# Optimization experiments

Measured on AMD Instinct MI355X. Metric: run time of the kernel, lower is better.

Reference implementation:

```python
import jax, jax.numpy as jnp
import numpy as np

NUM_HEADS = 8

def setup_inputs() -> dict:
    key = jax.random.key(0)
    ks = jax.random.split(key, 16)
    B, N, M, C = 4, 2048, 2048, 256
    Hd = 4 * C  # mlp hidden = dim * mlp_ratio
    std = 0.02
    x = jax.random.normal(ks[0], (B, N, C), dtype=jnp.float32)
    y = jax.random.normal(ks[1], (B, M, C), dtype=jnp.float32)
    token_types = jax.random.randint(ks[2], (B, N), 0, 2).astype(jnp.int64)
    token_types = token_types.at[0, 0].set(0)  # take the fresh-kv branch
    inp = {
        'x': x, 'y': y, 'token_types': token_types,
        'Wq': jax.random.normal(ks[3], (C, C)) * std,
        'Wkv': jax.random.normal(ks[4], (C, 2 * C)) * std,
        'Ws1': jax.random.normal(ks[5], (C, Hd)) * std,
        'bs1': jnp.zeros((Hd,)),
        'Ws2': jax.random.normal(ks[6], (Hd, C)) * std,
        'bs2': jnp.zeros((C,)),
        'Wl1': jax.random.normal(ks[7], (C, Hd)) * std,
        'bl1': jnp.zeros((Hd,)),
        'Wl2': jax.random.normal(ks[8], (Hd, C)) * std,
        'bl2': jnp.zeros((C,)),
    }
    return inp


def reference(x, y, token_types, Wq, Wkv, Ws1, bs1, Ws2, bs2, Wl1, bl1, Wl2, bl2):
    B, N, C = x.shape
    H = NUM_HEADS
    d = C // H
    scale = d ** -0.5
    # q: [B,H,N,d]
    q = (x @ Wq).reshape(B, N, H, d).transpose(0, 2, 1, 3)
    # kv: [B,M,2,H,d] -> k,v: [B,H,M,d]
    M = y.shape[1]
    kv = (y @ Wkv).reshape(B, M, 2, H, d)
    k = kv[:, :, 0].transpose(0, 2, 1, 3)
    v = kv[:, :, 1].transpose(0, 2, 1, 3)
    attn = jax.nn.softmax(jnp.einsum('bhnd,bhmd->bhnm', q, k) * scale, axis=-1)
    ctx = jnp.einsum('bhnm,bhmd->bhnd', attn, v)  # [B,H,N,d]
    ctx = ctx.transpose(0, 2, 1, 3).reshape(B, N, C)
    # MoE MLP: expert_s for token_type==0, expert_l for token_type==1
    out_s = jax.nn.gelu(ctx @ Ws1 + bs1, approximate=False) @ Ws2 + bs2
    out_l = jax.nn.gelu(ctx @ Wl1 + bl1, approximate=False) @ Wl2 + bl2
    is_l = (token_types == 1)[..., None]
    out = jnp.where(is_l, out_l, out_s)
    return out
```

## Files before the change

### kernel.cpp

```cpp
#include <hip/hip_runtime.h>

typedef unsigned short ushort_t;
typedef __attribute__((ext_vector_type(8))) short bf16x8;
typedef __attribute__((ext_vector_type(4))) short bf16x4;
typedef __attribute__((ext_vector_type(4))) float f32x4;

#define MFMA16(a, b, c) __builtin_amdgcn_mfma_f32_16x16x32_bf16(a, b, c, 0, 0, 0)

typedef const __attribute__((address_space(1))) void gvoid_t;
typedef __attribute__((address_space(3))) void lvoid_t;

__device__ __forceinline__ void glds16(const ushort_t* g, ushort_t* l) {
    __builtin_amdgcn_global_load_lds((gvoid_t*)(const void*)g, (lvoid_t*)(void*)l, 16, 0, 0);
}

__device__ inline ushort_t f2bf(float f) {
    union { float f; unsigned int i; } v;
    v.f = f;
    unsigned int r = v.i + 0x7FFFu + ((v.i >> 16) & 1u);
    return (ushort_t)(r >> 16);
}

__device__ __forceinline__ unsigned int cvtpk_bf16(float lo, float hi) {
    unsigned int r;
    asm("v_cvt_pk_bf16_f32 %0, %1, %2" : "=v"(r) : "v"(lo), "v"(hi));
    return r;
}

__device__ __forceinline__ float fexp2(float x) {
    float r;
    asm("v_exp_f32 %0, %1" : "=v"(r) : "v"(x));
    return r;
}

__device__ __forceinline__ float gelu_fast(float x) {
    float z = x * 0.70710678118654752f;
    float a = fabsf(z);
    float den = 1.0f + 0.3275911f * a;
    float tr;
    asm("v_rcp_f32 %0, %1" : "=v"(tr) : "v"(den));
    float poly = ((((1.061405429f * tr - 1.453152027f) * tr + 1.421413741f) * tr
                   - 0.284496736f) * tr + 0.254829592f) * tr;
    float e = fexp2(-z * z * 1.4426950408889634f);
    float erfa = 1.0f - poly * e;
    float erfv = copysignf(erfa, z);
    return 0.5f * x * (1.0f + erfv);
}

__global__ __launch_bounds__(256) void prep_k(
    const float* Wq, const float* Wkv, const float* Ws1,
    const float* Ws2, const float* Wl1, const float* Wl2,
    const float* x, const float* y, const int* tt,
    ushort_t* WqT, ushort_t* WkvT, ushort_t* Ws1T,
    ushort_t* Ws2T, ushort_t* Wl1T, ushort_t* Wl2T,
    ushort_t* xb, ushort_t* yb,
    int* perm0, int* perm1, int* cnt)
{
    const int job = blockIdx.y;
    const int t = threadIdx.x;
    if (job < 6) {
        __shared__ ushort_t lds[64][65];
        const float* src; ushort_t* dst; int R, Cc;
        switch (job) {
            case 0:  src = Wq;  dst = WqT;  R = 256;  Cc = 256;  break;
            case 1:  src = Wkv; dst = WkvT; R = 256;  Cc = 512;  break;
            case 2:  src = Ws1; dst = Ws1T; R = 256;  Cc = 1024; break;
            case 3:  src = Ws2; dst = Ws2T; R = 1024; Cc = 256;  break;
            case 4:  src = Wl1; dst = Wl1T; R = 256;  Cc = 1024; break;
            default: src = Wl2; dst = Wl2T; R = 1024; Cc = 256;  break;
        }
        const int ctiles = Cc >> 6;
        const int ntiles = (R >> 6) * ctiles;
        for (int tile = blockIdx.x; tile < ntiles; tile += gridDim.x) {
            const int r0 = (tile / ctiles) << 6, c0 = (tile - (tile / ctiles) * ctiles) << 6;
            #pragma unroll
            for (int it = 0; it < 16; ++it) {
                int idx = it * 256 + t;
                int rr = idx >> 6, cc = idx & 63;
                lds[rr][cc] = f2bf(src[(size_t)(r0 + rr) * Cc + c0 + cc]);
            }
            __syncthreads();
            #pragma unroll
            for (int it = 0; it < 16; ++it) {
                int idx = it * 256 + t;
                int rr = idx >> 6, cc = idx & 63;
                dst[(size_t)(c0 + rr) * R + r0 + cc] = lds[cc][rr];
            }
            __syncthreads();
        }
    } else if (job < 8) {
        const float* src = (job == 6) ? x : y;
        ushort_t* dst = (job == 6) ? xb : yb;
        const int tid = blockIdx.x * 256 + t;
        const int nth = gridDim.x * 256;
        for (int i = tid; i < (1 << 18); i += nth) {
            f32x4 a0 = *(const f32x4*)(src + (size_t)i * 8);
            f32x4 a1 = *(const f32x4*)(src + (size_t)i * 8 + 4);
            union { unsigned int u[4]; bf16x8 v; } o;
            o.u[0] = cvtpk_bf16(a0[0], a0[1]);
            o.u[1] = cvtpk_bf16(a0[2], a0[3]);
            o.u[2] = cvtpk_bf16(a1[0], a1[1]);
            o.u[3] = cvtpk_bf16(a1[2], a1[3]);
            *(bf16x8*)(dst + (size_t)i * 8) = o.v;
        }
    } else {
        if (blockIdx.x != 0) return;
        __shared__ int s0[256], s1[256];
        unsigned int mask = 0;
        #pragma unroll
        for (int j = 0; j < 8; ++j) {
            int4 v = *(const int4*)(tt + t * 32 + j * 4);
            mask |= (unsigned int)(v.x & 1) << (j * 4)
                  | (unsigned int)(v.y & 1) << (j * 4 + 1)
                  | (unsigned int)(v.z & 1) << (j * 4 + 2)
                  | (unsigned int)(v.w & 1) << (j * 4 + 3);
        }
        const int c1 = __popc(mask), c0 = 32 - c1;
        s0[t] = c0; s1[t] = c1;
        __syncthreads();
        for (int d = 1; d < 256; d <<= 1) {
            int a0 = 0, a1 = 0;
            if (t >= d) { a0 = s0[t - d]; a1 = s1[t - d]; }
            __syncthreads();
            s0[t] += a0; s1[t] += a1;
            __syncthreads();
        }
        const int tot0 = s0[255], tot1 = s1[255];
        int off0 = s0[t] - c0, off1 = s1[t] - c1;
        #pragma unroll
        for (int j = 0; j < 32; ++j) {
            int row = t * 32 + j;
            if ((mask >> j) & 1) perm1[off1++] = row;
            else                 perm0[off0++] = row;
        }
        for (int i = tot0 + t; i < 8320; i += 256) perm0[i] = 0;
        for (int i = tot1 + t; i < 8320; i += 256) perm1[i] = 0;
        if (t == 0) { cnt[0] = tot0; cnt[1] = tot1; }
    }
}

template<int ACT, int GATHER, int SCATTER, int OUTF32, int VSCATTER>
__device__ __forceinline__ void gemm_body(
    ushort_t* Als, ushort_t* Bls, int vbid,
    const ushort_t* __restrict__ A, const ushort_t* __restrict__ Bt,
    const float* __restrict__ bias, void* __restrict__ Cv,
    const int* __restrict__ perm, const int* __restrict__ ncnt,
    ushort_t* __restrict__ kpk, ushort_t* __restrict__ vpk,
    float oscale, int M, int N, int K, int aRowOff, int outRowOff)
{
    const int t = threadIdx.x;
    const int lane = t & 63, w = t >> 6;
    const int wr = w >> 1, wc = w & 1;
    const int ntn = N >> 7;
    const int mt = vbid / ntn, nt = vbid - mt * ntn;
    const int mbase = mt << 7, nbase = nt << 7;
    const int n16 = lane & 15, g = lane >> 4;

    int ne = M;
    if (GATHER || SCATTER) {
        ne = *ncnt;
        if (mbase >= ne) return;
    }

    int arow[4], skb[4], brow[4];
    #pragma unroll
    for (int j = 0; j < 4; ++j) {
        int p = j * 256 + t;
        int sr = p >> 3;
        skb[j] = (p & 7) ^ (sr & 7);
        brow[j] = sr;
        arow[j] = GATHER ? perm[mbase + sr] : (mbase + sr + aRowOff);
    }

    f32x4 acc[4][4];
    #pragma unroll
    for (int mi = 0; mi < 4; ++mi)
        #pragma unroll
        for (int ni = 0; ni < 4; ++ni) acc[mi][ni] = (f32x4){0.f, 0.f, 0.f, 0.f};

    for (int k0 = 0; k0 < K; k0 += 64) {
        #pragma unroll
        for (int j = 0; j < 4; ++j) {
            glds16(A + (size_t)arow[j] * K + k0 + skb[j] * 8, &Als[(j * 256 + t) * 8]);
            glds16(Bt + (size_t)(nbase + brow[j]) * K + k0 + skb[j] * 8, &Bls[(j * 256 + t) * 8]);
        }
        __syncthreads();
        #pragma unroll
        for (int ks = 0; ks < 2; ++ks) {
            bf16x8 af[4], bfr[4];
            #pragma unroll
            for (int i = 0; i < 4; ++i) {
                const int ar = wr * 64 + i * 16 + n16;
                af[i]  = *(const bf16x8*)&Als[ar * 64 + (((ks << 2) + g) ^ (ar & 7)) * 8];
                const int br = wc * 64 + i * 16 + n16;
                bfr[i] = *(const bf16x8*)&Bls[br * 64 + (((ks << 2) + g) ^ (br & 7)) * 8];
            }
            #pragma unroll
            for (int mi = 0; mi < 4; ++mi)
                #pragma unroll
                for (int ni = 0; ni < 4; ++ni)
                    acc[mi][ni] = MFMA16(af[mi], bfr[ni], acc[mi][ni]);
        }
        __syncthreads();
    }

    float bv[4];
    #pragma unroll
    for (int ni = 0; ni < 4; ++ni)
        bv[ni] = (bias != nullptr) ? bias[nbase + wc * 64 + ni * 16 + n16] : 0.f;

    #pragma unroll
    for (int mi = 0; mi < 4; ++mi) {
        #pragma unroll
        for (int r = 0; r < 4; ++r) {
            const int pos = mbase + wr * 64 + mi * 16 + (g << 2) + r;
            int orow = pos + outRowOff;
            if (GATHER || SCATTER) {
                if (pos >= ne) continue;
                if (SCATTER) orow = perm[pos];
            }
            #pragma unroll
            for (int ni = 0; ni < 4; ++ni) {
                const int col = nbase + wc * 64 + ni * 16 + n16;
                float v = (acc[mi][ni][r] + bv[ni]) * oscale;
                if (ACT) v = gelu_fast(v);
                if (VSCATTER) {
                    const int bb = pos >> 11, mm = pos & 2047;
                    if (col < 256) {
                        const int hh = col >> 5, dd = col & 31;
                        kpk[(size_t)(bb * 8 + hh) * 65536 + (mm >> 6) * 2048
                            + ((mm >> 4) & 3) * 512
                            + (((dd >> 3) * 16 + (mm & 15)) << 3) + (dd & 7)] = f2bf(v);
                    } else {
                        const int hh = (col - 256) >> 5, dd = (col - 256) & 31;
                        const int m31 = mm & 31;
                        vpk[(size_t)(bb * 8 + hh) * 65536 + (mm >> 6) * 2048
                            + (((mm >> 5) & 1) * 2 + (dd >> 4)) * 512
                            + ((((m31 >> 2) & 3) * 16 + (dd & 15)) << 3)
                            + (((m31 >> 4) & 1) << 2) + (m31 & 3)] = f2bf(v);
                    }
                } else {
                    if (OUTF32) ((float*)Cv)[(size_t)orow * N + col] = v;
                    else ((ushort_t*)Cv)[(size_t)orow * N + col] = f2bf(v);
                }
            }
        }
    }
}

__global__ __launch_bounds__(256, 2) void qkv_k(
    const ushort_t* xb, const ushort_t* yb,
    const ushort_t* WqT, const ushort_t* WkvT,
    ushort_t* qws, ushort_t* kpk, ushort_t* vpk, float qscale)
{
    __shared__ ushort_t Als[128 * 64];
    __shared__ ushort_t Bls[128 * 64];
    if (blockIdx.x < 128) {
        gemm_body<0, 0, 0, 0, 0>(Als, Bls, blockIdx.x, xb, WqT, nullptr, qws,
                                 nullptr, nullptr, nullptr, nullptr,
                                 qscale, 8192, 256, 256, 0, 0);
    } else {
        gemm_body<0, 0, 0, 0, 1>(Als, Bls, blockIdx.x - 128, yb, WkvT, nullptr, nullptr,
                                 nullptr, nullptr, kpk, vpk,
                                 1.f, 8192, 512, 256, 0, 0);
    }
}

__global__ __launch_bounds__(256, 2) void mlp1_k(
    const ushort_t* ctx, const ushort_t* Ws1T, const ushort_t* Wl1T,
    const float* bs1, const float* bl1, ushort_t* hws,
    const int* perm0, const int* perm1, const int* cnt)
{
    __shared__ ushort_t Als[128 * 64];
    __shared__ ushort_t Bls[128 * 64];
    const int half = blockIdx.x >> 9, vbid = blockIdx.x & 511;
    const int outOff = half ? cnt[0] : 0;
    gemm_body<1, 1, 0, 0, 0>(Als, Bls, vbid, ctx, half ? Wl1T : Ws1T,
                             half ? bl1 : bs1, hws,
                             half ? perm1 : perm0, cnt + half, nullptr, nullptr,
                             1.f, 8192, 1024, 256, 0, outOff);
}

__global__ __launch_bounds__(256, 2) void mlp2_k(
    const ushort_t* hws, const ushort_t* Ws2T, const ushort_t* Wl2T,
    const float* bs2, const float* bl2, float* out,
    const int* perm0, const int* perm1, const int* cnt)
{
    __shared__ ushort_t Als[128 * 64];
    __shared__ ushort_t Bls[128 * 64];
    const int half = blockIdx.x >> 7, vbid = blockIdx.x & 127;
    const int aOff = half ? cnt[0] : 0;
    gemm_body<0, 0, 1, 1, 0>(Als, Bls, vbid, hws, half ? Wl2T : Ws2T,
                             half ? bl2 : bs2, out,
                             half ? perm1 : perm0, cnt + half, nullptr, nullptr,
                             1.f, 8192, 256, 1024, aOff, 0);
}

__global__ __launch_bounds__(256, 3) void attn_k(
    const ushort_t* __restrict__ q, const ushort_t* __restrict__ kpack,
    const ushort_t* __restrict__ vpack, ushort_t* __restrict__ ctx)
{
    __shared__ ushort_t KV[2][4096];

    const int t = threadIdx.x, lane = t & 63, w = t >> 6;
    const int bid = (blockIdx.x & 7) * 64 + (blockIdx.x >> 3);
    const int tile = bid & 15, bh = bid >> 4, b = bh >> 3, h = bh & 7;
    const int n16 = lane & 15, g = lane >> 4, lk = g << 3;
    const int row0 = tile * 128 + w * 32;

    const ushort_t* qp = q + ((size_t)(b * 2048 + row0 + n16) * 256 + h * 32 + lk);
    const bf16x8 qf0 = *(const bf16x8*)qp;
    const bf16x8 qf1 = *(const bf16x8*)(qp + 16 * 256);

    const ushort_t* kg = kpack + (size_t)bh * 65536 + t * 8;
    const ushort_t* vg = vpack + (size_t)bh * 65536 + t * 8;

    f32x4 a0d0 = {0.f, 0.f, 0.f, 0.f}, a0d1 = {0.f, 0.f, 0.f, 0.f};
    f32x4 a1d0 = {0.f, 0.f, 0.f, 0.f}, a1d1 = {0.f, 0.f, 0.f, 0.f};
    f32x4 den0 = {0.f, 0.f, 0.f, 0.f}, den1 = {0.f, 0.f, 0.f, 0.f};
    const f32x4 zero = {0.f, 0.f, 0.f, 0.f};
    bf16x8 ones;
    #pragma unroll
    for (int e = 0; e < 8; ++e) ones[e] = (short)0x3F80;

    const int kOff = lane * 8;
    const int vOff = 2048 + lane * 8;

    bf16x8 kreg = *(const bf16x8*)kg;
    bf16x8 vreg = *(const bf16x8*)vg;
    *(bf16x8*)&KV[0][t * 8] = kreg;
    *(bf16x8*)&KV[0][2048 + t * 8] = vreg;

    int cur = 0;
    for (int it = 0; it < 32; ++it) {
        __syncthreads();
        if (it + 1 < 32) {
            kreg = *(const bf16x8*)(kg + (size_t)(it + 1) * 2048);
            vreg = *(const bf16x8*)(vg + (size_t)(it + 1) * 2048);
        }

        bf16x8 kf[4], vf[4];
        #pragma unroll
        for (int i = 0; i < 4; ++i) {
            kf[i] = *(const bf16x8*)&KV[cur][kOff + i * 512];
            vf[i] = *(const bf16x8*)&KV[cur][vOff + i * 512];
        }

        f32x4 st0[4], st1[4];
        __builtin_amdgcn_s_setprio(1);
        #pragma unroll
        for (int mt = 0; mt < 4; ++mt) {
            st0[mt] = MFMA16(kf[mt], qf0, zero);
            st1[mt] = MFMA16(kf[mt], qf1, zero);
        }
        __builtin_amdgcn_s_setprio(0);

        float p0[4][4], p1[4][4];
        #pragma unroll
        for (int mt = 0; mt < 4; ++mt) {
            #pragma unroll
            for (int r = 0; r < 4; ++r) {
                p0[mt][r] = fexp2(st0[mt][r]);
                p1[mt][r] = fexp2(st1[mt][r]);
            }
        }

        __builtin_amdgcn_s_setprio(1);
        #pragma unroll
        for (int kpn = 0; kpn < 2; ++kpn) {
            union { unsigned int u[4]; bf16x8 v; } pb0, pb1;
            pb0.u[0] = cvtpk_bf16(p0[2 * kpn][0], p0[2 * kpn][1]);
            pb0.u[1] = cvtpk_bf16(p0[2 * kpn][2], p0[2 * kpn][3]);
            pb0.u[2] = cvtpk_bf16(p0[2 * kpn + 1][0], p0[2 * kpn + 1][1]);
            pb0.u[3] = cvtpk_bf16(p0[2 * kpn + 1][2], p0[2 * kpn + 1][3]);
            pb1.u[0] = cvtpk_bf16(p1[2 * kpn][0], p1[2 * kpn][1]);
            pb1.u[1] = cvtpk_bf16(p1[2 * kpn][2], p1[2 * kpn][3]);
            pb1.u[2] = cvtpk_bf16(p1[2 * kpn + 1][0], p1[2 * kpn + 1][1]);
            pb1.u[3] = cvtpk_bf16(p1[2 * kpn + 1][2], p1[2 * kpn + 1][3]);
            a0d0 = MFMA16(vf[2 * kpn],     pb0.v, a0d0);
            a0d1 = MFMA16(vf[2 * kpn + 1], pb0.v, a0d1);
            a1d0 = MFMA16(vf[2 * kpn],     pb1.v, a1d0);
            a1d1 = MFMA16(vf[2 * kpn + 1], pb1.v, a1d1);
            den0 = MFMA16(ones, pb0.v, den0);
            den1 = MFMA16(ones, pb1.v, den1);
        }
        __builtin_amdgcn_s_setprio(0);

        if (it + 1 < 32) {
            *(bf16x8*)&KV[cur ^ 1][t * 8] = kreg;
            *(bf16x8*)&KV[cur ^ 1][2048 + t * 8] = vreg;
        }
        cur ^= 1;
    }

    const float i0 = 1.f / den0[0], i1 = 1.f / den1[0];
    bf16x4 s00, s01, s10, s11;
    #pragma unroll
    for (int r = 0; r < 4; ++r) {
        s00[r] = (short)f2bf(a0d0[r] * i0);
        s01[r] = (short)f2bf(a0d1[r] * i0);
        s10[r] = (short)f2bf(a1d0[r] * i1);
        s11[r] = (short)f2bf(a1d1[r] * i1);
    }
    ushort_t* op0 = ctx + (size_t)(b * 2048 + row0 + n16) * 256 + h * 32;
    ushort_t* op1 = op0 + 16 * 256;
    *(bf16x4*)(op0 + 4 * g)      = s00;
    *(bf16x4*)(op0 + 16 + 4 * g) = s01;
    *(bf16x4*)(op1 + 4 * g)      = s10;
    *(bf16x4*)(op1 + 16 + 4 * g) = s11;
}

extern "C" void kernel_launch(void* const* d_in, const int* in_sizes, int n_in,
                              void* d_out, int out_size, void* d_ws, size_t ws_size,
                              hipStream_t stream)
{
    const float* x   = (const float*)d_in[0];
    const float* y   = (const float*)d_in[1];
    const int*   tt  = (const int*)d_in[2];
    const float* Wq  = (const float*)d_in[3];
    const float* Wkv = (const float*)d_in[4];
    const float* Ws1 = (const float*)d_in[5];
    const float* bs1 = (const float*)d_in[6];
    const float* Ws2 = (const float*)d_in[7];
    const float* bs2 = (const float*)d_in[8];
    const float* Wl1 = (const float*)d_in[9];
    const float* bl1 = (const float*)d_in[10];
    const float* Wl2 = (const float*)d_in[11];
    const float* bl2 = (const float*)d_in[12];
    float* out = (float*)d_out;
    ushort_t* ws = (ushort_t*)d_ws;

    ushort_t* WqT   = ws;
    ushort_t* WkvT  = WqT  + 65536;
    ushort_t* Ws1T  = WkvT + 131072;
    ushort_t* Ws2T  = Ws1T + 262144;
    ushort_t* Wl1T  = Ws2T + 262144;
    ushort_t* Wl2T  = Wl1T + 262144;
    ushort_t* kpws  = Wl2T + 262144;
    ushort_t* vtws  = kpws + (size_t)8192 * 512;
    ushort_t* ctxws = vtws + 2097152;
    ushort_t* regA  = ctxws + 2097152;
    ushort_t* xbf   = regA;
    ushort_t* ybf   = xbf + 2097152;
    ushort_t* qws   = ybf + 2097152;
    ushort_t* hws   = regA;
    int* iws   = (int*)(ws + (size_t)18022400);
    int* perm0 = iws;
    int* perm1 = iws + 8320;
    int* cnt   = iws + 16640;

    const float qscale = 0.17677669529663687f * 1.4426950408889634f;

    prep_k<<<dim3(64, 9), 256, 0, stream>>>(Wq, Wkv, Ws1, Ws2, Wl1, Wl2, x, y, tt,
                                            WqT, WkvT, Ws1T, Ws2T, Wl1T, Wl2T,
                                            xbf, ybf, perm0, perm1, cnt);

    qkv_k<<<dim3(384), 256, 0, stream>>>(xbf, ybf, WqT, WkvT, qws, kpws, vtws, qscale);

    attn_k<<<dim3(512), 256, 0, stream>>>(qws, kpws, vtws, ctxws);

    mlp1_k<<<dim3(1024), 256, 0, stream>>>(ctxws, Ws1T, Wl1T, bs1, bl1, hws,
                                           perm0, perm1, cnt);
    mlp2_k<<<dim3(256), 256, 0, stream>>>(hws, Ws2T, Wl2T, bs2, bl2, out,
                                          perm0, perm1, cnt);
}
```

Baseline: 90.96 us.

## Split attention over two key halves and merge partials in a combine kernel

The attention kernel now splits each (batch, head, query tile) job into two halves of the key range. This doubles the grid from 512 to 1024 blocks, so the GPU has more blocks in flight, and the occupancy hint rises from 3 to 4 blocks per CU. Each half writes a bf16 context normalised by its own denominator, plus the raw denominators. A new combine kernel reweights the two partials by their denominators and divides by their sum. The cost is an extra kernel launch, extra global traffic for the partial contexts, and a small rounding error from the bf16 intermediates.

```diff
diff --git a/kernel.cpp b/kernel.cpp
--- a/kernel.cpp
+++ b/kernel.cpp
@@ -12,6 +12,12 @@
 
 __device__ __forceinline__ void glds16(const ushort_t* g, ushort_t* l) {
     __builtin_amdgcn_global_load_lds((gvoid_t*)(const void*)g, (lvoid_t*)(void*)l, 16, 0, 0);
+}
+
+__device__ inline float bf2f(ushort_t u) {
+    union { unsigned int i; float f; } v;
+    v.i = ((unsigned int)u) << 16;
+    return v.f;
 }
 
 __device__ inline ushort_t f2bf(float f) {
@@ -296,15 +302,17 @@
                              1.f, 8192, 256, 1024, aOff, 0);
 }
 
-__global__ __launch_bounds__(256, 3) void attn_k(
+__global__ __launch_bounds__(256, 4) void attn_k(
     const ushort_t* __restrict__ q, const ushort_t* __restrict__ kpack,
-    const ushort_t* __restrict__ vpack, ushort_t* __restrict__ ctx)
+    const ushort_t* __restrict__ vpack, ushort_t* __restrict__ pctx,
+    float* __restrict__ dens)
 {
     __shared__ ushort_t KV[2][4096];
 
     const int t = threadIdx.x, lane = t & 63, w = t >> 6;
-    const int bid = (blockIdx.x & 7) * 64 + (blockIdx.x >> 3);
-    const int tile = bid & 15, bh = bid >> 4, b = bh >> 3, h = bh & 7;
+    const int bid = (blockIdx.x & 7) * 128 + (blockIdx.x >> 3);
+    const int bh = bid >> 5, rem = bid & 31, tile = rem >> 1, split = rem & 1;
+    const int b = bh >> 3, h = bh & 7;
     const int n16 = lane & 15, g = lane >> 4, lk = g << 3;
     const int row0 = tile * 128 + w * 32;
 
@@ -312,8 +320,8 @@
     const bf16x8 qf0 = *(const bf16x8*)qp;
     const bf16x8 qf1 = *(const bf16x8*)(qp + 16 * 256);
 
-    const ushort_t* kg = kpack + (size_t)bh * 65536 + t * 8;
-    const ushort_t* vg = vpack + (size_t)bh * 65536 + t * 8;
+    const ushort_t* kg = kpack + (size_t)bh * 65536 + split * 32768 + t * 8;
+    const ushort_t* vg = vpack + (size_t)bh * 65536 + split * 32768 + t * 8;
 
     f32x4 a0d0 = {0.f, 0.f, 0.f, 0.f}, a0d1 = {0.f, 0.f, 0.f, 0.f};
     f32x4 a1d0 = {0.f, 0.f, 0.f, 0.f}, a1d1 = {0.f, 0.f, 0.f, 0.f};
@@ -323,18 +331,15 @@
     #pragma unroll
     for (int e = 0; e < 8; ++e) ones[e] = (short)0x3F80;
 
-    const int kOff = lane * 8;
-    const int vOff = 2048 + lane * 8;
-
     bf16x8 kreg = *(const bf16x8*)kg;
     bf16x8 vreg = *(const bf16x8*)vg;
     *(bf16x8*)&KV[0][t * 8] = kreg;
     *(bf16x8*)&KV[0][2048 + t * 8] = vreg;
 
     int cur = 0;
-    for (int it = 0; it < 32; ++it) {
+    for (int it = 0; it < 16; ++it) {
         __syncthreads();
-        if (it + 1 < 32) {
+        if (it + 1 < 16) {
             kreg = *(const bf16x8*)(kg + (size_t)(it + 1) * 2048);
             vreg = *(const bf16x8*)(vg + (size_t)(it + 1) * 2048);
         }
@@ -342,8 +347,8 @@
         bf16x8 kf[4], vf[4];
         #pragma unroll
         for (int i = 0; i < 4; ++i) {
-            kf[i] = *(const bf16x8*)&KV[cur][kOff + i * 512];
-            vf[i] = *(const bf16x8*)&KV[cur][vOff + i * 512];
+            kf[i] = *(const bf16x8*)&KV[cur][lane * 8 + i * 512];
+            vf[i] = *(const bf16x8*)&KV[cur][2048 + lane * 8 + i * 512];
         }
 
         f32x4 st0[4], st1[4];
@@ -386,7 +391,7 @@
         }
         __builtin_amdgcn_s_setprio(0);
 
-        if (it + 1 < 32) {
+        if (it + 1 < 16) {
             *(bf16x8*)&KV[cur ^ 1][t * 8] = kreg;
             *(bf16x8*)&KV[cur ^ 1][2048 + t * 8] = vreg;
         }
@@ -402,12 +407,39 @@
         s10[r] = (short)f2bf(a1d0[r] * i1);
         s11[r] = (short)f2bf(a1d1[r] * i1);
     }
-    ushort_t* op0 = ctx + (size_t)(b * 2048 + row0 + n16) * 256 + h * 32;
+    ushort_t* op0 = pctx + (size_t)split * 2097152
+                  + (size_t)(b * 2048 + row0 + n16) * 256 + h * 32;
     ushort_t* op1 = op0 + 16 * 256;
     *(bf16x4*)(op0 + 4 * g)      = s00;
     *(bf16x4*)(op0 + 16 + 4 * g) = s01;
     *(bf16x4*)(op1 + 4 * g)      = s10;
     *(bf16x4*)(op1 + 16 + 4 * g) = s11;
+    if (g == 0) {
+        dens[split * 16384 + (b * 2048 + row0 + n16) * 8 + h]      = den0[0];
+        dens[split * 16384 + (b * 2048 + row0 + 16 + n16) * 8 + h] = den1[0];
+    }
+}
+
+__global__ __launch_bounds__(256) void combine_k(
+    const ushort_t* __restrict__ pctx, const float* __restrict__ dens,
+    ushort_t* __restrict__ ctx)
+{
+    for (int i = blockIdx.x * 256 + threadIdx.x; i < 8192 * 64; i += gridDim.x * 256) {
+        const int row = i >> 6, c4 = (i & 63) << 2, h = c4 >> 5;
+        const float dA = dens[row * 8 + h];
+        const float dB = dens[16384 + row * 8 + h];
+        float inv;
+        asm("v_rcp_f32 %0, %1" : "=v"(inv) : "v"(dA + dB));
+        const size_t off = (size_t)row * 256 + c4;
+        bf16x4 a = *(const bf16x4*)(pctx + off);
+        bf16x4 bb = *(const bf16x4*)(pctx + 2097152 + off);
+        bf16x4 o;
+        #pragma unroll
+        for (int j = 0; j < 4; ++j)
+            o[j] = (short)f2bf((bf2f((ushort_t)a[j]) * dA
+                              + bf2f((ushort_t)bb[j]) * dB) * inv);
+        *(bf16x4*)(ctx + off) = o;
+    }
 }
 
 extern "C" void kernel_launch(void* const* d_in, const int* in_sizes, int n_in,
@@ -443,6 +475,8 @@
     ushort_t* xbf   = regA;
     ushort_t* ybf   = xbf + 2097152;
     ushort_t* qws   = ybf + 2097152;
+    ushort_t* pctx  = regA;
+    float*    dens  = (float*)(regA + 6291456);
     ushort_t* hws   = regA;
     int* iws   = (int*)(ws + (size_t)18022400);
     int* perm0 = iws;
@@ -457,7 +491,8 @@
 
     qkv_k<<<dim3(384), 256, 0, stream>>>(xbf, ybf, WqT, WkvT, qws, kpws, vtws, qscale);
 
-    attn_k<<<dim3(512), 256, 0, stream>>>(qws, kpws, vtws, ctxws);
+    attn_k<<<dim3(1024), 256, 0, stream>>>(qws, kpws, vtws, pctx, dens);
+    combine_k<<<dim3(1024), 256, 0, stream>>>(pctx, dens, ctxws);
 
     mlp1_k<<<dim3(1024), 256, 0, stream>>>(ctxws, Ws1T, Wl1T, bs1, bl1, hws,
                                            perm0, perm1, cnt);
```

After: 95.32 us. 1.05x slower.
